# Kernel optimization log

Hardware: AMD Instinct MI355X
Metric: run time of the kernel (lower is better)

Reference implementation:

```python
import jax, jax.numpy as jnp
import numpy as np

EMB, HID, KEY, VAL, VOCAB = 400, 300, 128, 128, 33
T, B, S = 256, 256, 512


def setup_inputs() -> dict:
    key = jax.random.key(0)
    ks = jax.random.split(key, 12)
    sc = 0.05
    return {
        "input": jax.random.randint(ks[0], (T, B), 0, VOCAB),
        "keys": jax.random.normal(ks[1], (S, B, KEY), jnp.float32),
        "values": jax.random.normal(ks[2], (S, B, VAL), jnp.float32),
        "embedding": jax.random.normal(ks[3], (VOCAB, EMB), jnp.float32) * sc,
        "phi_w": jax.random.normal(ks[4], (KEY, HID), jnp.float32) * sc,
        "phi_b": jnp.zeros((KEY,), jnp.float32),
        "h0": jnp.zeros((1, HID), jnp.float32),
        "c0": jnp.zeros((1, HID), jnp.float32),
        "W_ih": jax.random.normal(ks[5], (4 * HID, EMB + VAL), jnp.float32) * sc,
        "b_ih": jnp.zeros((4 * HID,), jnp.float32),
        "W_hh": jax.random.normal(ks[6], (4 * HID, HID), jnp.float32) * sc,
        "b_hh": jnp.zeros((4 * HID,), jnp.float32),
        "proj_w": jax.random.normal(ks[7], (VOCAB, HID + VAL), jnp.float32) * sc,
        "proj_b": jnp.zeros((VOCAB,), jnp.float32),
    }


def _attend(h, phi_w, phi_b, keys, values):
    # query: [B,KEY]; keys: [S,B,KEY]; values: [S,B,VAL]
    q = h @ phi_w.T + phi_b
    energy = jnp.einsum('bk,sbk->bs', q, keys)
    att = jax.nn.softmax(energy, axis=-1)
    return jnp.einsum('bs,sbd->bd', att, values)


def reference(input, keys, values, embedding, phi_w, phi_b, h0, c0,
              W_ih, b_ih, W_hh, b_hh, proj_w, proj_b):
    Bb = input.shape[1]
    h = jnp.broadcast_to(h0, (Bb, h0.shape[1]))
    c = jnp.broadcast_to(c0, (Bb, c0.shape[1]))
    ctx = _attend(h, phi_w, phi_b, keys, values)

    def step(carry, x_t):
        h, c, ctx = carry
        emb = embedding[x_t]                       # [B,EMB]
        xin = jnp.concatenate([emb, ctx], axis=-1)  # [B,EMB+VAL]
        gates = xin @ W_ih.T + b_ih + h @ W_hh.T + b_hh
        i, f, g, o = jnp.split(gates, 4, axis=-1)
        c = jax.nn.sigmoid(f) * c + jax.nn.sigmoid(i) * jnp.tanh(g)
        h = jax.nn.sigmoid(o) * jnp.tanh(c)
        logits = jnp.concatenate([h, ctx], axis=-1) @ proj_w.T + proj_b
        ctx = _attend(h, phi_w, phi_b, keys, values)
        return (h, c, ctx), logits

    _, logit_list = jax.lax.scan(step, (h, c, ctx), input)
    return logit_list  # [T,B,VOCAB]
```

## Files before the change

kernel.cpp:

```cpp
#include <hip/hip_runtime.h>
#include <math.h>

#define EMBD 400
#define HIDD 300
#define KEYD 128
#define VALD 128
#define NVOC 33
#define TT 256
#define BB 256
#define SS 512
#define WIH_LD 528
#define GDIM 1200
#define KTOT 428
#define KPAD 432
#define NK2 216
#define NI2 152
#define NBLK 256

typedef unsigned int u32;
typedef unsigned int u32x4 __attribute__((ext_vector_type(4)));
typedef _Float16 f16x2 __attribute__((ext_vector_type(2)));

__device__ __forceinline__ f16x2 h2u(u32 u) {
    return __builtin_bit_cast(f16x2, u);
}
__device__ __forceinline__ float fdot2_(u32 w, f16x2 x, float c) {
    return __builtin_amdgcn_fdot2(h2u(w), x, c, false);
}
__device__ __forceinline__ float sigmoidf_(float x) {
    return 1.f / (1.f + __expf(-x));
}
__device__ __forceinline__ float tanh_f(float x) {
    float ax = fabsf(x);
    if (ax > 15.f) return x > 0.f ? 1.f : -1.f;
    float e = __expf(2.f * x);
    return (e - 1.f) / (e + 1.f);
}

__global__ __launch_bounds__(256) void p_e2(
    const float* __restrict__ emb, const float* __restrict__ Wih,
    const float* __restrict__ bih, const float* __restrict__ bhh,
    float* __restrict__ E2)
{
    __shared__ float es[EMBD];
    const int v = blockIdx.x;
    for (int i = threadIdx.x; i < EMBD; i += 256) es[i] = emb[v * EMBD + i];
    __syncthreads();
    for (int j = threadIdx.x; j < GDIM; j += 256) {
        const float* wr = &Wih[(size_t)j * WIH_LD];
        float s0 = 0.f, s1 = 0.f, s2 = 0.f, s3 = 0.f;
        for (int e = 0; e < EMBD; e += 4) {
            s0 += es[e]     * wr[e];
            s1 += es[e + 1] * wr[e + 1];
            s2 += es[e + 2] * wr[e + 2];
            s3 += es[e + 3] * wr[e + 3];
        }
        E2[v * GDIM + j] = bih[j] + bhh[j] + ((s0 + s1) + (s2 + s3));
    }
}

__global__ __launch_bounds__(256) void p_w2(
    const float* __restrict__ Wih, const float* __restrict__ Whh,
    const float* __restrict__ phi_w,
    u32* __restrict__ W2, u32* __restrict__ phi2)
{
    const int stride = gridDim.x * 256;
    const int tot1 = NK2 * GDIM;
    for (int m = blockIdx.x * 256 + threadIdx.x; m < tot1; m += stride) {
        int k2 = m / GDIM, j = m - k2 * GDIM;
        float w0 = 0.f, w1 = 0.f;
        int k0 = 2 * k2, k1 = 2 * k2 + 1;
        if (k0 < KEYD)      w0 = Wih[(size_t)j * WIH_LD + EMBD + k0];
        else if (k0 < KTOT) w0 = Whh[(size_t)j * HIDD + (k0 - KEYD)];
        if (k1 < KEYD)      w1 = Wih[(size_t)j * WIH_LD + EMBD + k1];
        else if (k1 < KTOT) w1 = Whh[(size_t)j * HIDD + (k1 - KEYD)];
        f16x2 p; p[0] = (_Float16)w0; p[1] = (_Float16)w1;
        W2[m] = __builtin_bit_cast(u32, p);
    }
    const int tot2 = NI2 * KEYD;
    for (int m = blockIdx.x * 256 + threadIdx.x; m < tot2; m += stride) {
        int i2 = m >> 7, k = m & 127;
        float w0 = 0.f, w1 = 0.f;
        if (2 * i2 < HIDD)     w0 = phi_w[(size_t)k * HIDD + 2 * i2];
        if (2 * i2 + 1 < HIDD) w1 = phi_w[(size_t)k * HIDD + 2 * i2 + 1];
        f16x2 p; p[0] = (_Float16)w0; p[1] = (_Float16)w1;
        phi2[m] = __builtin_bit_cast(u32, p);
    }
}

__global__ __launch_bounds__(1024) void p_kv(
    const float* __restrict__ keys, const float* __restrict__ values,
    _Float16* __restrict__ kh, _Float16* __restrict__ vh2)
{
    size_t i = (size_t)blockIdx.x * 1024 + threadIdx.x;
    int s = (int)(i >> 15);
    int r = (int)(i & 32767);
    int b = r >> 7, d = r & 127;
    kh[(((size_t)b * SS + s) << 7) + d] = (_Float16)keys[i];
    size_t vd = ((((size_t)b * 256 + (s >> 1)) << 7) + d) * 2 + (s & 1);
    vh2[vd] = (_Float16)values[i];
}

__device__ __forceinline__ void logits33(
    int tid, int b, int t, const float* __restrict__ projw,
    const float* __restrict__ projb, float* __restrict__ out,
    const float* __restrict__ h_s, const float* __restrict__ ctx_s)
{
    if (tid >= 512) {
        const int idx = tid - 512;
        const int l = idx & 15;
        const int vs = idx >> 4;
        #pragma unroll
        for (int rep = 0; rep < 2; ++rep) {
            const int v = vs + rep * 32;
            if (v < NVOC) {
                const float* pw = projw + (size_t)v * KTOT;
                float s = 0.f;
                for (int k = l; k < KTOT; k += 16) {
                    float u = (k < HIDD) ? h_s[k] : ctx_s[k - HIDD];
                    s += pw[k] * u;
                }
                #pragma unroll
                for (int off = 8; off; off >>= 1) s += __shfl_xor(s, off);
                if (l == 0)
                    out[((size_t)t * BB + b) * NVOC + v] = s + projb[v];
            }
        }
    }
}

template<int OVL>
__device__ __forceinline__ void attend1(
    const int tid, const int b, const int t,
    const _Float16* __restrict__ kh, const _Float16* __restrict__ vh2,
    const u32* __restrict__ phi2, const float* __restrict__ phi_b,
    const float* __restrict__ projw, const float* __restrict__ projb,
    float* __restrict__ out,
    float* h_s, float* ctx_s, float* q_s, float* att, _Float16* att_h,
    float (*qp)[KEYD], float (*cpart)[VALD], float* redM, float* redS,
    _Float16* xinh, const u32* xin2)
{
    if (tid < 512) {
        const int k = tid & 127, sl = tid >> 7;
        const int i20 = sl * 38;
        float acc = 0.f;
        #pragma unroll 19
        for (int i2 = i20; i2 < i20 + 38; ++i2)
            acc = fdot2_(phi2[i2 * 128 + k], h2u(xin2[64 + i2]), acc);
        qp[sl][k] = acc;
    } else if (OVL) {
        logits33(tid, b, t, projw, projb, out, h_s, ctx_s);
    }
    __syncthreads();
    if (tid < KEYD)
        q_s[tid] = phi_b[tid] + qp[0][tid] + qp[1][tid] + qp[2][tid] + qp[3][tid];
    __syncthreads();

    {
        const int l16 = tid & 15, sg = tid >> 4;
        const float4* q4 = reinterpret_cast<const float4*>(q_s);
        const float4 qa = q4[l16 * 2], qb = q4[l16 * 2 + 1];
        f16x2 q2a, q2b, q2c, q2d;
        q2a[0] = (_Float16)qa.x; q2a[1] = (_Float16)qa.y;
        q2b[0] = (_Float16)qa.z; q2b[1] = (_Float16)qa.w;
        q2c[0] = (_Float16)qb.x; q2c[1] = (_Float16)qb.y;
        q2d[0] = (_Float16)qb.z; q2d[1] = (_Float16)qb.w;
        const _Float16* krow = kh + (((size_t)b * SS) << 7);
        #pragma unroll
        for (int p = 0; p < 8; ++p) {
            int s = p * 64 + sg;
            const u32x4* kp = reinterpret_cast<const u32x4*>(krow + ((size_t)s << 7));
            u32x4 w = __builtin_nontemporal_load(kp + l16);
            float e = fdot2_(w.x, q2a, 0.f);
            e = fdot2_(w.y, q2b, e);
            e = fdot2_(w.z, q2c, e);
            e = fdot2_(w.w, q2d, e);
            e += __shfl_xor(e, 1);
            e += __shfl_xor(e, 2);
            e += __shfl_xor(e, 4);
            e += __shfl_xor(e, 8);
            if (l16 == 0) att[s] = e;
        }
    }
    __syncthreads();

    {
        const int lane = tid & 63, wv = tid >> 6;
        float e0 = (tid < 512) ? att[tid] : -1e30f;
        float m = e0;
        #pragma unroll
        for (int off = 32; off; off >>= 1) m = fmaxf(m, __shfl_xor(m, off));
        if (tid < 512 && lane == 0) redM[wv] = m;
        __syncthreads();
        float M = redM[0];
        #pragma unroll
        for (int w = 1; w < 8; ++w) M = fmaxf(M, redM[w]);
        float p0 = (tid < 512) ? __expf(e0 - M) : 0.f;
        float ss = p0;
        #pragma unroll
        for (int off = 32; off; off >>= 1) ss += __shfl_xor(ss, off);
        if (tid < 512 && lane == 0) redS[wv] = ss;
        __syncthreads();
        float inv = 1.f / (redS[0] + redS[1] + redS[2] + redS[3]
                         + redS[4] + redS[5] + redS[6] + redS[7]);
        if (tid < 512) {
            float pv = p0 * inv;
            att[tid] = pv;
            att_h[tid] = (_Float16)pv;
        }
    }
    __syncthreads();

    {
        const int v4 = tid & 31, sg = tid >> 5;
        float4 a = make_float4(0.f, 0.f, 0.f, 0.f);
        const u32* vrow = reinterpret_cast<const u32*>(vh2) + (((size_t)b * 256) << 7);
        const u32* att2 = reinterpret_cast<const u32*>(att_h);
        #pragma unroll
        for (int i = 0; i < 8; ++i) {
            int s2 = sg * 8 + i;
            f16x2 wt2 = h2u(att2[s2]);
            const u32x4* vp = reinterpret_cast<const u32x4*>(vrow + ((size_t)s2 << 7));
            u32x4 w = __builtin_nontemporal_load(vp + v4);
            a.x = fdot2_(w.x, wt2, a.x);
            a.y = fdot2_(w.y, wt2, a.y);
            a.z = fdot2_(w.z, wt2, a.z);
            a.w = fdot2_(w.w, wt2, a.w);
        }
        *reinterpret_cast<float4*>(&cpart[sg][v4 * 4]) = a;
    }
    __syncthreads();
    if (tid < VALD) {
        float s = 0.f;
        #pragma unroll
        for (int g = 0; g < 32; ++g) s += cpart[g][tid];
        ctx_s[tid] = s;
        xinh[tid] = (_Float16)s;
    }
    __syncthreads();
}

__global__ void __launch_bounds__(1024, 4) decoder_dot(
    const int* __restrict__ input,
    const _Float16* __restrict__ kh, const _Float16* __restrict__ vh2,
    const u32* __restrict__ phi2, const float* __restrict__ phi_b,
    const float* __restrict__ h0, const float* __restrict__ c0,
    const float* __restrict__ projw, const float* __restrict__ projb,
    const float* __restrict__ E2, const u32* __restrict__ W2,
    float* __restrict__ out)
{
    const int tid = threadIdx.x;
    const int b = blockIdx.x;

    __shared__ float h_s[HIDD];
    __shared__ float c_s[HIDD];
    __shared__ float ctx_s[VALD];
    __shared__ __align__(16) _Float16 xinh[448];
    __shared__ __align__(16) float gp[3 * GDIM];
    __shared__ __align__(16) float att[SS];
    __shared__ __align__(16) _Float16 att_h[SS];
    __shared__ __align__(16) float q_s[KEYD];
    __shared__ __align__(16) float qp[4][KEYD];
    __shared__ __align__(16) float cpart[32][VALD];
    __shared__ float redM[8], redS[8];
    __shared__ int xv_s;

    const u32* xin2 = reinterpret_cast<const u32*>(xinh);

    for (int j = tid; j < HIDD; j += 1024) {
        float hv = h0[j];
        h_s[j] = hv;
        c_s[j] = c0[j];
        xinh[VALD + j] = (_Float16)hv;
    }
    if (tid < 448 - KTOT) xinh[KTOT + tid] = (_Float16)0.f;
    __syncthreads();

    attend1<0>(tid, b, 0, kh, vh2, phi2, phi_b, projw, projb, out,
               h_s, ctx_s, q_s, att, att_h, qp, cpart, redM, redS, xinh, xin2);

    #pragma unroll 1
    for (int t = 0; t < TT; ++t) {
        if (tid < 900) {
            const int c = tid / 300;
            const int q = tid - c * 300;
            const u32* Wp = W2 + (size_t)(c * 72) * GDIM + 4 * q;
            const u32* xp = xin2 + c * 72;
            float a0 = 0.f, a1 = 0.f, a2 = 0.f, a3 = 0.f;
            #pragma unroll 8
            for (int k2 = 0; k2 < 72; ++k2) {
                f16x2 x2 = h2u(xp[k2]);
                u32x4 w = *reinterpret_cast<const u32x4*>(Wp + (size_t)k2 * GDIM);
                a0 = fdot2_(w.x, x2, a0);
                a1 = fdot2_(w.y, x2, a1);
                a2 = fdot2_(w.z, x2, a2);
                a3 = fdot2_(w.w, x2, a3);
            }
            reinterpret_cast<float4*>(gp + c * GDIM)[q] =
                make_float4(a0, a1, a2, a3);
        } else if (tid == 1023) {
            xv_s = input[t * BB + b];
        }
        __syncthreads();

        if (tid < HIDD) {
            const int j = tid;
            const float* e2r = E2 + (size_t)xv_s * GDIM;
            float gi = gp[j]
                     + gp[GDIM + j]
                     + gp[2 * GDIM + j]            + e2r[j];
            float gf = gp[HIDD + j]
                     + gp[GDIM + HIDD + j]
                     + gp[2 * GDIM + HIDD + j]     + e2r[HIDD + j];
            float gg = gp[2 * HIDD + j]
                     + gp[GDIM + 2 * HIDD + j]
                     + gp[2 * GDIM + 2 * HIDD + j] + e2r[2 * HIDD + j];
            float go = gp[3 * HIDD + j]
                     + gp[GDIM + 3 * HIDD + j]
                     + gp[2 * GDIM + 3 * HIDD + j] + e2r[3 * HIDD + j];
            float ig = sigmoidf_(gi);
            float fg = sigmoidf_(gf);
            float gt = tanh_f(gg);
            float og = sigmoidf_(go);
            float cn = fg * c_s[j] + ig * gt;
            c_s[j] = cn;
            float hv = og * tanh_f(cn);
            h_s[j] = hv;
            xinh[VALD + j] = (_Float16)hv;
        }
        __syncthreads();

        if (t < TT - 1) {
            attend1<1>(tid, b, t, kh, vh2, phi2, phi_b, projw, projb, out,
                       h_s, ctx_s, q_s, att, att_h, qp, cpart, redM, redS,
                       xinh, xin2);
        } else {
            logits33(tid, b, t, projw, projb, out, h_s, ctx_s);
        }
    }
}

extern "C" void kernel_launch(void* const* d_in, const int* in_sizes, int n_in,
                              void* d_out, int out_size, void* d_ws, size_t ws_size,
                              hipStream_t stream)
{
    const int*   input     = (const int*)  d_in[0];
    const float* keys      = (const float*)d_in[1];
    const float* values    = (const float*)d_in[2];
    const float* embedding = (const float*)d_in[3];
    const float* phi_w     = (const float*)d_in[4];
    const float* phi_b     = (const float*)d_in[5];
    const float* h0        = (const float*)d_in[6];
    const float* c0        = (const float*)d_in[7];
    const float* W_ih      = (const float*)d_in[8];
    const float* b_ih      = (const float*)d_in[9];
    const float* W_hh      = (const float*)d_in[10];
    const float* b_hh      = (const float*)d_in[11];
    const float* proj_w    = (const float*)d_in[12];
    const float* proj_b    = (const float*)d_in[13];
    float* out = (float*)d_out;

    char* base = (char*)d_ws;
    size_t off = 0;
    auto alloc = [&](size_t bytes) {
        size_t o = off;
        off = (off + bytes + 255) & ~(size_t)255;
        return o;
    };
    size_t oE2   = alloc((size_t)NVOC * GDIM * 4);
    size_t oPhi  = alloc((size_t)NI2 * KEYD * 4);
    size_t oW2   = alloc((size_t)NK2 * GDIM * 4);
    size_t oKh   = alloc((size_t)BB * SS * KEYD * 2);
    size_t oVh   = alloc((size_t)BB * SS * VALD * 2);
    (void)off;

    float* E2    = (float*)(base + oE2);
    u32* phi2    = (u32*)(base + oPhi);
    u32* W2      = (u32*)(base + oW2);
    _Float16* kh = (_Float16*)(base + oKh);
    _Float16* vh2= (_Float16*)(base + oVh);

    p_e2<<<NVOC, 256, 0, stream>>>(embedding, W_ih, b_ih, b_hh, E2);
    p_w2<<<2048, 256, 0, stream>>>(W_ih, W_hh, phi_w, W2, phi2);
    p_kv<<<(SS * BB * KEYD) / 1024, 1024, 0, stream>>>(keys, values, kh, vh2);

    decoder_dot<<<NBLK, 1024, 0, stream>>>(
        input, kh, vh2, phi2, phi_b, h0, c0,
        proj_w, proj_b, E2, W2, out);
}
```

Before: 6.382 ms.

## Cut barriers in attention step, prefetch values, single-wave softmax

New measurement: 8.256 ms. +29.4%, slower.

```diff
diff --git a/kernel.cpp b/kernel.cpp
--- a/kernel.cpp
+++ b/kernel.cpp
@@ -27,6 +27,10 @@
 __device__ __forceinline__ float fdot2_(u32 w, f16x2 x, float c) {
     return __builtin_amdgcn_fdot2(h2u(w), x, c, false);
 }
+__device__ __forceinline__ u32 packh2(float a, float b) {
+    f16x2 p; p[0] = (_Float16)a; p[1] = (_Float16)b;
+    return __builtin_bit_cast(u32, p);
+}
 __device__ __forceinline__ float sigmoidf_(float x) {
     return 1.f / (1.f + __expf(-x));
 }
@@ -74,8 +78,7 @@
         else if (k0 < KTOT) w0 = Whh[(size_t)j * HIDD + (k0 - KEYD)];
         if (k1 < KEYD)      w1 = Wih[(size_t)j * WIH_LD + EMBD + k1];
         else if (k1 < KTOT) w1 = Whh[(size_t)j * HIDD + (k1 - KEYD)];
-        f16x2 p; p[0] = (_Float16)w0; p[1] = (_Float16)w1;
-        W2[m] = __builtin_bit_cast(u32, p);
+        W2[m] = packh2(w0, w1);
     }
     const int tot2 = NI2 * KEYD;
     for (int m = blockIdx.x * 256 + threadIdx.x; m < tot2; m += stride) {
@@ -83,8 +86,7 @@
         float w0 = 0.f, w1 = 0.f;
         if (2 * i2 < HIDD)     w0 = phi_w[(size_t)k * HIDD + 2 * i2];
         if (2 * i2 + 1 < HIDD) w1 = phi_w[(size_t)k * HIDD + 2 * i2 + 1];
-        f16x2 p; p[0] = (_Float16)w0; p[1] = (_Float16)w1;
-        phi2[m] = __builtin_bit_cast(u32, p);
+        phi2[m] = packh2(w0, w1);
     }
 }
 
@@ -133,11 +135,11 @@
 __device__ __forceinline__ void attend1(
     const int tid, const int b, const int t,
     const _Float16* __restrict__ kh, const _Float16* __restrict__ vh2,
-    const u32* __restrict__ phi2, const float* __restrict__ phi_b,
+    const u32* __restrict__ phi2, const float* __restrict__ pb_s,
     const float* __restrict__ projw, const float* __restrict__ projb,
     float* __restrict__ out,
-    float* h_s, float* ctx_s, float* q_s, float* att, _Float16* att_h,
-    float (*qp)[KEYD], float (*cpart)[VALD], float* redM, float* redS,
+    float* h_s, float* ctx_s, float* att, u32* att2,
+    float (*qp)[KEYD], float (*cpart)[VALD],
     _Float16* xinh, const u32* xin2)
 {
     if (tid < 512) {
@@ -152,14 +154,25 @@
         logits33(tid, b, t, projw, projb, out, h_s, ctx_s);
     }
     __syncthreads();
-    if (tid < KEYD)
-        q_s[tid] = phi_b[tid] + qp[0][tid] + qp[1][tid] + qp[2][tid] + qp[3][tid];
-    __syncthreads();
-
+
+    u32x4 vpre[8];
     {
         const int l16 = tid & 15, sg = tid >> 4;
-        const float4* q4 = reinterpret_cast<const float4*>(q_s);
-        const float4 qa = q4[l16 * 2], qb = q4[l16 * 2 + 1];
+        const int ia = l16 * 2, ib = ia + 1;
+        const float4* pb4 = reinterpret_cast<const float4*>(pb_s);
+        const float4* q0 = reinterpret_cast<const float4*>(qp[0]);
+        const float4* q1 = reinterpret_cast<const float4*>(qp[1]);
+        const float4* q2 = reinterpret_cast<const float4*>(qp[2]);
+        const float4* q3 = reinterpret_cast<const float4*>(qp[3]);
+        float4 qa, qb;
+        qa.x = pb4[ia].x + q0[ia].x + q1[ia].x + q2[ia].x + q3[ia].x;
+        qa.y = pb4[ia].y + q0[ia].y + q1[ia].y + q2[ia].y + q3[ia].y;
+        qa.z = pb4[ia].z + q0[ia].z + q1[ia].z + q2[ia].z + q3[ia].z;
+        qa.w = pb4[ia].w + q0[ia].w + q1[ia].w + q2[ia].w + q3[ia].w;
+        qb.x = pb4[ib].x + q0[ib].x + q1[ib].x + q2[ib].x + q3[ib].x;
+        qb.y = pb4[ib].y + q0[ib].y + q1[ib].y + q2[ib].y + q3[ib].y;
+        qb.z = pb4[ib].z + q0[ib].z + q1[ib].z + q2[ib].z + q3[ib].z;
+        qb.w = pb4[ib].w + q0[ib].w + q1[ib].w + q2[ib].w + q3[ib].w;
         f16x2 q2a, q2b, q2c, q2d;
         q2a[0] = (_Float16)qa.x; q2a[1] = (_Float16)qa.y;
         q2b[0] = (_Float16)qa.z; q2b[1] = (_Float16)qa.w;
@@ -170,7 +183,7 @@
         for (int p = 0; p < 8; ++p) {
             int s = p * 64 + sg;
             const u32x4* kp = reinterpret_cast<const u32x4*>(krow + ((size_t)s << 7));
-            u32x4 w = __builtin_nontemporal_load(kp + l16);
+            u32x4 w = kp[l16];
             float e = fdot2_(w.x, q2a, 0.f);
             e = fdot2_(w.y, q2b, e);
             e = fdot2_(w.z, q2c, e);
@@ -182,52 +195,52 @@
             if (l16 == 0) att[s] = e;
         }
     }
-    __syncthreads();
-
     {
-        const int lane = tid & 63, wv = tid >> 6;
-        float e0 = (tid < 512) ? att[tid] : -1e30f;
-        float m = e0;
+        const int v4 = tid & 31, sg5 = tid >> 5;
+        const u32* vrow = reinterpret_cast<const u32*>(vh2) + (((size_t)b * 256) << 7);
+        #pragma unroll
+        for (int i = 0; i < 8; ++i) {
+            const u32x4* vp = reinterpret_cast<const u32x4*>(
+                vrow + ((size_t)(sg5 * 8 + i) << 7));
+            vpre[i] = vp[v4];
+        }
+    }
+    __syncthreads();
+
+    if (tid < 64) {
+        const float4* a4 = reinterpret_cast<const float4*>(att);
+        float4 e0 = a4[tid * 2], e1 = a4[tid * 2 + 1];
+        float m = fmaxf(fmaxf(fmaxf(e0.x, e0.y), fmaxf(e0.z, e0.w)),
+                        fmaxf(fmaxf(e1.x, e1.y), fmaxf(e1.z, e1.w)));
         #pragma unroll
         for (int off = 32; off; off >>= 1) m = fmaxf(m, __shfl_xor(m, off));
-        if (tid < 512 && lane == 0) redM[wv] = m;
-        __syncthreads();
-        float M = redM[0];
-        #pragma unroll
-        for (int w = 1; w < 8; ++w) M = fmaxf(M, redM[w]);
-        float p0 = (tid < 512) ? __expf(e0 - M) : 0.f;
-        float ss = p0;
+        float p0 = __expf(e0.x - m), p1 = __expf(e0.y - m);
+        float p2 = __expf(e0.z - m), p3 = __expf(e0.w - m);
+        float p4 = __expf(e1.x - m), p5 = __expf(e1.y - m);
+        float p6 = __expf(e1.z - m), p7 = __expf(e1.w - m);
+        float ss = ((p0 + p1) + (p2 + p3)) + ((p4 + p5) + (p6 + p7));
         #pragma unroll
         for (int off = 32; off; off >>= 1) ss += __shfl_xor(ss, off);
-        if (tid < 512 && lane == 0) redS[wv] = ss;
-        __syncthreads();
-        float inv = 1.f / (redS[0] + redS[1] + redS[2] + redS[3]
-                         + redS[4] + redS[5] + redS[6] + redS[7]);
-        if (tid < 512) {
-            float pv = p0 * inv;
-            att[tid] = pv;
-            att_h[tid] = (_Float16)pv;
-        }
+        float inv = 1.f / ss;
+        att2[tid * 4 + 0] = packh2(p0 * inv, p1 * inv);
+        att2[tid * 4 + 1] = packh2(p2 * inv, p3 * inv);
+        att2[tid * 4 + 2] = packh2(p4 * inv, p5 * inv);
+        att2[tid * 4 + 3] = packh2(p6 * inv, p7 * inv);
     }
     __syncthreads();
 
     {
-        const int v4 = tid & 31, sg = tid >> 5;
+        const int v4 = tid & 31, sg5 = tid >> 5;
         float4 a = make_float4(0.f, 0.f, 0.f, 0.f);
-        const u32* vrow = reinterpret_cast<const u32*>(vh2) + (((size_t)b * 256) << 7);
-        const u32* att2 = reinterpret_cast<const u32*>(att_h);
         #pragma unroll
         for (int i = 0; i < 8; ++i) {
-            int s2 = sg * 8 + i;
-            f16x2 wt2 = h2u(att2[s2]);
-            const u32x4* vp = reinterpret_cast<const u32x4*>(vrow + ((size_t)s2 << 7));
-            u32x4 w = __builtin_nontemporal_load(vp + v4);
-            a.x = fdot2_(w.x, wt2, a.x);
-            a.y = fdot2_(w.y, wt2, a.y);
-            a.z = fdot2_(w.z, wt2, a.z);
-            a.w = fdot2_(w.w, wt2, a.w);
-        }
-        *reinterpret_cast<float4*>(&cpart[sg][v4 * 4]) = a;
+            f16x2 wt2 = h2u(att2[sg5 * 8 + i]);
+            a.x = fdot2_(vpre[i].x, wt2, a.x);
+            a.y = fdot2_(vpre[i].y, wt2, a.y);
+            a.z = fdot2_(vpre[i].z, wt2, a.z);
+            a.w = fdot2_(vpre[i].w, wt2, a.w);
+        }
+        *reinterpret_cast<float4*>(&cpart[sg5][v4 * 4]) = a;
     }
     __syncthreads();
     if (tid < VALD) {
@@ -258,12 +271,11 @@
     __shared__ __align__(16) _Float16 xinh[448];
     __shared__ __align__(16) float gp[3 * GDIM];
     __shared__ __align__(16) float att[SS];
-    __shared__ __align__(16) _Float16 att_h[SS];
-    __shared__ __align__(16) float q_s[KEYD];
+    __shared__ __align__(16) u32 att2[SS / 2];
     __shared__ __align__(16) float qp[4][KEYD];
     __shared__ __align__(16) float cpart[32][VALD];
-    __shared__ float redM[8], redS[8];
-    __shared__ int xv_s;
+    __shared__ __align__(16) float pb_s[KEYD];
+    __shared__ int xcol[TT];
 
     const u32* xin2 = reinterpret_cast<const u32*>(xinh);
 
@@ -274,10 +286,12 @@
         xinh[VALD + j] = (_Float16)hv;
     }
     if (tid < 448 - KTOT) xinh[KTOT + tid] = (_Float16)0.f;
-    __syncthreads();
-
-    attend1<0>(tid, b, 0, kh, vh2, phi2, phi_b, projw, projb, out,
-               h_s, ctx_s, q_s, att, att_h, qp, cpart, redM, redS, xinh, xin2);
+    if (tid < KEYD) pb_s[tid] = phi_b[tid];
+    if (tid >= 512 && tid < 512 + TT) xcol[tid - 512] = input[(tid - 512) * BB + b];
+    __syncthreads();
+
+    attend1<0>(tid, b, 0, kh, vh2, phi2, pb_s, projw, projb, out,
+               h_s, ctx_s, att, att2, qp, cpart, xinh, xin2);
 
     #pragma unroll 1
     for (int t = 0; t < TT; ++t) {
@@ -298,14 +312,12 @@
             }
             reinterpret_cast<float4*>(gp + c * GDIM)[q] =
                 make_float4(a0, a1, a2, a3);
-        } else if (tid == 1023) {
-            xv_s = input[t * BB + b];
         }
         __syncthreads();
 
         if (tid < HIDD) {
             const int j = tid;
-            const float* e2r = E2 + (size_t)xv_s * GDIM;
+            const float* e2r = E2 + (size_t)xcol[t] * GDIM;
             float gi = gp[j]
                      + gp[GDIM + j]
                      + gp[2 * GDIM + j]            + e2r[j];
@@ -331,9 +343,8 @@
         __syncthreads();
 
         if (t < TT - 1) {
-            attend1<1>(tid, b, t, kh, vh2, phi2, phi_b, projw, projb, out,
-                       h_s, ctx_s, q_s, att, att_h, qp, cpart, redM, redS,
-                       xinh, xin2);
+            attend1<1>(tid, b, t, kh, vh2, phi2, pb_s, projw, projb, out,
+                       h_s, ctx_s, att, att2, qp, cpart, xinh, xin2);
         } else {
             logits33(tid, b, t, projw, projb, out, h_s, ctx_s);
         }
```
